# Kernel optimization log

Measured on AMD Instinct MI355X. Metric: run time of the kernel, lower is better.

Reference implementation:

```python
import jax, jax.numpy as jnp
import numpy as np

N = 50000        # nodes
E = 1600000      # edges (avg degree 32)
N_IN = 128       # atomic embedding dim
N_F = 128        # filter dim
N_G = 50         # gaussian basis size for fij
CUTOFF = 5.0


def setup_inputs() -> dict:
    key = jax.random.key(0)
    ks = jax.random.split(key, 12)
    feat = jax.random.normal(ks[0], (N, N_IN), jnp.float32)
    fij = jax.random.uniform(ks[1], (E, N_G), dtype=jnp.float32)
    rij = jax.random.uniform(ks[2], (E,), dtype=jnp.float32) * CUTOFF
    src = jax.random.randint(ks[3], (E,), 0, N, dtype=jnp.int32)
    dst = jax.random.randint(ks[4], (E,), 0, N, dtype=jnp.int32)

    def w(k, shape, fan_in):
        return jax.random.normal(k, shape, jnp.float32) / np.float32(np.sqrt(fan_in))

    W_in2f = w(ks[5], (N_IN, N_F), N_IN)                 # Dense(n_in, n_filters, bias=False)
    Wf1 = w(ks[6], (N_G, N_F), N_G); bf1 = jnp.zeros((N_F,), jnp.float32)   # filter_network layer 1 (swish)
    Wf2 = w(ks[7], (N_F, N_F), N_F); bf2 = jnp.zeros((N_F,), jnp.float32)   # filter_network layer 2
    Wm1 = w(ks[8], (N_F, N_IN), N_F); bm1 = jnp.zeros((N_IN,), jnp.float32) # msg_transform layer 1 (swish)
    Wm2 = w(ks[9], (N_IN, N_IN), N_IN); bm2 = jnp.zeros((N_IN,), jnp.float32)
    return dict(feat=feat, fij=fij, rij=rij, src=src, dst=dst,
                W_in2f=W_in2f, Wf1=Wf1, bf1=bf1, Wf2=Wf2, bf2=bf2,
                Wm1=Wm1, bm1=bm1, Wm2=Wm2, bm2=bm2)


def _swish(x):
    return x * jax.nn.sigmoid(x)


def reference(feat, fij, rij, src, dst, W_in2f, Wf1, bf1, Wf2, bf2, Wm1, bm1, Wm2, bm2):
    # Cosine cutoff: 0.5*(cos(pi*r/rc)+1) for r < rc, else 0
    C = 0.5 * (jnp.cos(jnp.pi * rij / CUTOFF) + 1.0) * (rij < CUTOFF).astype(rij.dtype)
    # Edge filters: filter_network(fij) * C  -> [E, n_filters]
    he = (_swish(fij @ Wf1 + bf1) @ Wf2 + bf2) * C[:, None]
    # Node features projected: in2f(feat) -> [N, n_filters]
    hv = feat @ W_in2f
    # u_mul_e: gather source node feature, multiply by edge filter -> [E, n_filters]
    m = hv[src] * he
    # aggregator: sum messages at destination nodes -> [N, n_filters]
    agg = jax.ops.segment_sum(m, dst, num_segments=N)
    # msg_transform: Dense(swish) -> Dense
    return _swish(agg @ Wm1 + bm1) @ Wm2 + bm2
```

## Files before the change

### kernel.cpp

```cpp
#include <hip/hip_runtime.h>

#define N_NODES 50000
#define N_EDGES 1600000

typedef _Float16 f16x8 __attribute__((ext_vector_type(8)));
typedef float f32x4 __attribute__((ext_vector_type(4)));

__global__ void prep_weights(const float* __restrict__ Wf1,
                             const float* __restrict__ Wf2,
                             _Float16* __restrict__ W1img,
                             _Float16* __restrict__ W2img) {
    int i = blockIdx.x * 256 + threadIdx.x;
    if (i < 8192) {
        int n = i >> 6, k = i & 63;
        float v = (k < 50) ? Wf1[k * 128 + n] : 0.0f;
        W1img[n * 64 + (((k >> 3) ^ (n & 7)) << 3) + (k & 7)] = (_Float16)v;
    }
    if (i < 16384) {
        int n = i >> 7, k = i & 127;
        W2img[n * 128 + (((k >> 3) ^ (n & 7)) << 3) + (k & 7)] =
            (_Float16)Wf2[k * 128 + n];
    }
}

__global__ void hist_kernel(const int* __restrict__ dstv, int* __restrict__ cnt) {
    int e = blockIdx.x * 256 + threadIdx.x;
    if (e < N_EDGES) atomicAdd(&cnt[dstv[e]], 1);
}

__global__ __launch_bounds__(1024) void scan_reduce(const int* __restrict__ cnt,
                                                    int* __restrict__ bsum) {
    __shared__ int ws[16];
    int tid = threadIdx.x, lane = tid & 63;
    int i = blockIdx.x * 1024 + tid;
    int x = (i < N_NODES) ? cnt[i] : 0;
    for (int o = 32; o > 0; o >>= 1) x += __shfl_down(x, o);
    if (lane == 0) ws[tid >> 6] = x;
    __syncthreads();
    if (tid == 0) {
        int s = 0;
        for (int w = 0; w < 16; ++w) s += ws[w];
        bsum[blockIdx.x] = s;
    }
}

__global__ void scan_top(int* __restrict__ bsum) {
    if (threadIdx.x == 0) {
        int s = 0;
        for (int b = 0; b < 49; ++b) { int v = bsum[b]; bsum[b] = s; s += v; }
    }
}

__global__ __launch_bounds__(1024) void scan_apply(int* __restrict__ cnt,
                                                   const int* __restrict__ bsum) {
    __shared__ int ws[16], wo[16];
    int tid = threadIdx.x, lane = tid & 63, wid = tid >> 6;
    int i = blockIdx.x * 1024 + tid;
    int x = (i < N_NODES) ? cnt[i] : 0;
    int incl = x;
    for (int o = 1; o < 64; o <<= 1) {
        int y = __shfl_up(incl, o);
        if (lane >= o) incl += y;
    }
    if (lane == 63) ws[wid] = incl;
    __syncthreads();
    if (tid == 0) {
        int s = 0;
        for (int w = 0; w < 16; ++w) { wo[w] = s; s += ws[w]; }
    }
    __syncthreads();
    if (i < N_NODES) cnt[i] = bsum[blockIdx.x] + wo[wid] + incl - x;
}

__global__ void scatter_kernel(const int* __restrict__ dstv,
                               const int* __restrict__ srcv,
                               const float* __restrict__ rij,
                               int* __restrict__ cursor,
                               int4* __restrict__ meta) {
    int e = blockIdx.x * 256 + threadIdx.x;
    if (e < N_EDGES) {
        int d = dstv[e];
        int pos = atomicAdd(&cursor[d], 1);
        meta[pos] = make_int4(e, srcv[e], d, __float_as_int(rij[e]));
    }
}

__global__ __launch_bounds__(256) void hv_kernel(const float* __restrict__ feat,
                                                 const float* __restrict__ W,
                                                 _Float16* __restrict__ hvh) {
    __shared__ float sAT[128 * 20];
    const int tid = threadIdx.x;
    const int row0 = blockIdx.x * 16;
    for (int t = 0; t < 8; ++t) {
        int flat = tid + 256 * t;
        int rr = flat >> 7, k = flat & 127;
        sAT[k * 20 + rr] = feat[(row0 + rr) * 128 + k];
    }
    __syncthreads();
    const int c = tid & 127, rh = tid >> 7;
    float acc[8] = {0, 0, 0, 0, 0, 0, 0, 0};
    for (int k = 0; k < 128; ++k) {
        float wval = W[k * 128 + c];
        const float4 alo = *(const float4*)&sAT[k * 20 + rh * 8];
        const float4 ahi = *(const float4*)&sAT[k * 20 + rh * 8 + 4];
        acc[0] += alo.x * wval; acc[1] += alo.y * wval;
        acc[2] += alo.z * wval; acc[3] += alo.w * wval;
        acc[4] += ahi.x * wval; acc[5] += ahi.y * wval;
        acc[6] += ahi.z * wval; acc[7] += ahi.w * wval;
    }
    for (int r = 0; r < 8; ++r)
        hvh[(row0 + rh * 8 + r) * 128 + c] = (_Float16)acc[r];
}

__global__ __launch_bounds__(512, 4) void edge_kernel(
        const float* __restrict__ fij, const _Float16* __restrict__ hvh,
        const _Float16* __restrict__ W1img, const _Float16* __restrict__ W2img,
        const float* __restrict__ bf1, const float* __restrict__ bf2,
        const int4* __restrict__ meta, float* __restrict__ agg) {
    __shared__ __align__(16) char smem[65536];
    __shared__ __align__(16) int4 sMeta[128];
    _Float16* sW1 = (_Float16*)smem;
    _Float16* sW2 = (_Float16*)(smem + 16384);
    _Float16* sT0 = (_Float16*)smem;
    _Float16* sT1 = (_Float16*)(smem + 49152);
    _Float16* sM  = (_Float16*)(smem + 16384);

    const int tid = threadIdx.x;
    const int lane = tid & 63;
    const int wv = tid >> 6;
    const int l15 = lane & 15;
    const int q = lane >> 4;
    const int e0 = blockIdx.x * 128;

    const int arow = wv * 16 + l15;
    const int eid = meta[e0 + arow].x;
    const float* frow = fij + (long)eid * 50;
    float2 p0 = *(const float2*)(frow + q * 8 + 0);
    float2 p1 = *(const float2*)(frow + q * 8 + 2);
    float2 p2 = *(const float2*)(frow + q * 8 + 4);
    float2 p3 = *(const float2*)(frow + q * 8 + 6);
    const int kb = 32 + q * 8;
    float2 z2 = make_float2(0.f, 0.f);
    float2 p4 = (kb + 1 < 50) ? *(const float2*)(frow + kb + 0) : z2;
    float2 p5 = (kb + 3 < 50) ? *(const float2*)(frow + kb + 2) : z2;
    float2 p6 = (kb + 5 < 50) ? *(const float2*)(frow + kb + 4) : z2;
    float2 p7 = (kb + 7 < 50) ? *(const float2*)(frow + kb + 6) : z2;
    f16x8 a0, a1;
    a0[0] = (_Float16)p0.x; a0[1] = (_Float16)p0.y;
    a0[2] = (_Float16)p1.x; a0[3] = (_Float16)p1.y;
    a0[4] = (_Float16)p2.x; a0[5] = (_Float16)p2.y;
    a0[6] = (_Float16)p3.x; a0[7] = (_Float16)p3.y;
    a1[0] = (_Float16)p4.x; a1[1] = (_Float16)p4.y;
    a1[2] = (_Float16)p5.x; a1[3] = (_Float16)p5.y;
    a1[4] = (_Float16)p6.x; a1[5] = (_Float16)p6.y;
    a1[6] = (_Float16)p7.x; a1[7] = (_Float16)p7.y;

    if (tid < 128) sMeta[tid] = meta[e0 + tid];
    {
        const float4* s1 = (const float4*)W1img;
        float4* d1 = (float4*)sW1;
        d1[tid] = s1[tid]; d1[tid + 512] = s1[tid + 512];
        const float4* s2 = (const float4*)W2img;
        float4* d2 = (float4*)sW2;
        for (int t = 0; t < 4; ++t) d2[tid + 512 * t] = s2[tid + 512 * t];
    }
    float b1v[8], b2v[8];
    for (int nb = 0; nb < 8; ++nb) {
        b1v[nb] = bf1[nb * 16 + l15];
        b2v[nb] = bf2[nb * 16 + l15];
    }
    __syncthreads();

    const int col2 = tid & 63;
    const int rseg0 = (tid >> 6) * 16;
    unsigned int pf[16];
    #pragma unroll
    for (int i = 0; i < 16; ++i) {
        long srcn = sMeta[rseg0 + i].y;
        pf[i] = *(const unsigned int*)(hvh + srcn * 128 + col2 * 2);
    }

    f32x4 acc[8];
    for (int nb = 0; nb < 8; ++nb) acc[nb] = (f32x4){0.f, 0.f, 0.f, 0.f};
    {
        f16x8 b[8];
        for (int nb = 0; nb < 8; ++nb) {
            int n = nb * 16 + l15;
            b[nb] = *(const f16x8*)&sW1[n * 64 + ((q ^ (n & 7)) << 3)];
        }
        for (int nb = 0; nb < 8; ++nb)
            acc[nb] = __builtin_amdgcn_mfma_f32_16x16x32_f16(a0, b[nb], acc[nb], 0, 0, 0);
        for (int nb = 0; nb < 8; ++nb) {
            int n = nb * 16 + l15;
            b[nb] = *(const f16x8*)&sW1[n * 64 + (((4 + q) ^ (n & 7)) << 3)];
        }
        for (int nb = 0; nb < 8; ++nb)
            acc[nb] = __builtin_amdgcn_mfma_f32_16x16x32_f16(a1, b[nb], acc[nb], 0, 0, 0);
    }
    __syncthreads();

    for (int nb = 0; nb < 8; ++nb)
        for (int r = 0; r < 4; ++r) {
            float x = acc[nb][r] + b1v[nb];
            float tt = x / (1.0f + __expf(-x));
            int row = wv * 16 + q * 4 + r;
            int col = nb * 16 + l15;
            _Float16* base = (row < 64) ? sT0 + row * 128 : sT1 + (row - 64) * 128;
            base[(((col >> 3) ^ (row & 7)) << 3) + (col & 7)] = (_Float16)tt;
        }
    __syncthreads();

    for (int nb = 0; nb < 8; ++nb) acc[nb] = (f32x4){0.f, 0.f, 0.f, 0.f};
    {
        const int row = wv * 16 + l15;
        const _Float16* abase = (row < 64) ? sT0 + row * 128 : sT1 + (row - 64) * 128;
        for (int ks = 0; ks < 4; ++ks) {
            int c = ks * 4 + q;
            f16x8 a = *(const f16x8*)&abase[(c ^ (row & 7)) << 3];
            for (int nb = 0; nb < 8; ++nb) {
                int n = nb * 16 + l15;
                f16x8 b = *(const f16x8*)&sW2[n * 128 + ((c ^ (n & 7)) << 3)];
                acc[nb] = __builtin_amdgcn_mfma_f32_16x16x32_f16(a, b, acc[nb], 0, 0, 0);
            }
        }
    }
    __syncthreads();

    for (int r = 0; r < 4; ++r) {
        int row = wv * 16 + q * 4 + r;
        float rv = __int_as_float(sMeta[row].w);
        float Cr = (rv < 5.0f) ? 0.5f * (__cosf(0.6283185307179586f * rv) + 1.0f) : 0.0f;
        for (int nb = 0; nb < 8; ++nb) {
            int col = nb * 16 + l15;
            sM[row * 132 + col] = (_Float16)((acc[nb][r] + b2v[nb]) * Cr);
        }
    }
    __syncthreads();

    {
        float run0 = 0.0f, run1 = 0.0f;
        int cur = sMeta[rseg0].z;
        #pragma unroll
        for (int i = 0; i < 16; ++i) {
            int r = rseg0 + i;
            int d = sMeta[r].z;
            if (d != cur) {
                atomicAdd(&agg[cur * 128 + col2 * 2], run0);
                atomicAdd(&agg[cur * 128 + col2 * 2 + 1], run1);
                run0 = 0.0f; run1 = 0.0f; cur = d;
            }
            union { unsigned int u; _Float16 h[2]; } hv2; hv2.u = pf[i];
            union { unsigned int u; _Float16 h[2]; } m2;
            m2.u = *(const unsigned int*)&sM[r * 132 + col2 * 2];
            run0 += (float)hv2.h[0] * (float)m2.h[0];
            run1 += (float)hv2.h[1] * (float)m2.h[1];
        }
        atomicAdd(&agg[cur * 128 + col2 * 2], run0);
        atomicAdd(&agg[cur * 128 + col2 * 2 + 1], run1);
    }
}

__global__ __launch_bounds__(256) void out_kernel(const float* __restrict__ agg,
                                                  const float* __restrict__ Wm1,
                                                  const float* __restrict__ bm1,
                                                  const float* __restrict__ Wm2,
                                                  const float* __restrict__ bm2,
                                                  float* __restrict__ out) {
    __shared__ float sAT[128 * 20];
    __shared__ float sTT[128 * 20];
    const int tid = threadIdx.x;
    const int row0 = blockIdx.x * 16;
    for (int t = 0; t < 8; ++t) {
        int flat = tid + 256 * t;
        int rr = flat >> 7, k = flat & 127;
        sAT[k * 20 + rr] = agg[(row0 + rr) * 128 + k];
    }
    __syncthreads();
    const int c = tid & 127, rh = tid >> 7;
    float acc[8] = {0, 0, 0, 0, 0, 0, 0, 0};
    for (int k = 0; k < 128; ++k) {
        float wval = Wm1[k * 128 + c];
        const float4 alo = *(const float4*)&sAT[k * 20 + rh * 8];
        const float4 ahi = *(const float4*)&sAT[k * 20 + rh * 8 + 4];
        acc[0] += alo.x * wval; acc[1] += alo.y * wval;
        acc[2] += alo.z * wval; acc[3] += alo.w * wval;
        acc[4] += ahi.x * wval; acc[5] += ahi.y * wval;
        acc[6] += ahi.z * wval; acc[7] += ahi.w * wval;
    }
    float bm1c = bm1[c];
    for (int r = 0; r < 8; ++r) {
        float x = acc[r] + bm1c;
        sTT[c * 20 + rh * 8 + r] = x / (1.0f + __expf(-x));
    }
    __syncthreads();
    float acc2[8] = {0, 0, 0, 0, 0, 0, 0, 0};
    for (int k = 0; k < 128; ++k) {
        float wval = Wm2[k * 128 + c];
        const float4 alo = *(const float4*)&sTT[k * 20 + rh * 8];
        const float4 ahi = *(const float4*)&sTT[k * 20 + rh * 8 + 4];
        acc2[0] += alo.x * wval; acc2[1] += alo.y * wval;
        acc2[2] += alo.z * wval; acc2[3] += alo.w * wval;
        acc2[4] += ahi.x * wval; acc2[5] += ahi.y * wval;
        acc2[6] += ahi.z * wval; acc2[7] += ahi.w * wval;
    }
    float bm2c = bm2[c];
    for (int r = 0; r < 8; ++r)
        out[(row0 + rh * 8 + r) * 128 + c] = acc2[r] + bm2c;
}

extern "C" void kernel_launch(void* const* d_in, const int* in_sizes, int n_in,
                              void* d_out, int out_size, void* d_ws, size_t ws_size,
                              hipStream_t stream) {
    const float* feat   = (const float*)d_in[0];
    const float* fij    = (const float*)d_in[1];
    const float* rij    = (const float*)d_in[2];
    const int*   srcv   = (const int*)d_in[3];
    const int*   dstv   = (const int*)d_in[4];
    const float* W_in2f = (const float*)d_in[5];
    const float* Wf1    = (const float*)d_in[6];
    const float* bf1    = (const float*)d_in[7];
    const float* Wf2    = (const float*)d_in[8];
    const float* bf2    = (const float*)d_in[9];
    const float* Wm1    = (const float*)d_in[10];
    const float* bm1    = (const float*)d_in[11];
    const float* Wm2    = (const float*)d_in[12];
    const float* bm2    = (const float*)d_in[13];
    float* out = (float*)d_out;

    char* ws = (char*)d_ws;
    float*    agg   = (float*)ws;
    _Float16* hvh   = (_Float16*)(ws + 25600000);
    int4*     meta  = (int4*)(ws + 38400000);
    int*      cnt   = (int*)(ws + 64000000);
    int*      bsum  = (int*)(ws + 64200000);
    _Float16* W1img = (_Float16*)(ws + 64200704);
    _Float16* W2img = (_Float16*)(ws + 64217088);

    hipMemsetAsync(agg, 0, (size_t)N_NODES * 128 * sizeof(float), stream);
    hipMemsetAsync(cnt, 0, (size_t)N_NODES * sizeof(int), stream);
    prep_weights<<<64, 256, 0, stream>>>(Wf1, Wf2, W1img, W2img);
    hv_kernel<<<3125, 256, 0, stream>>>(feat, W_in2f, hvh);
    hist_kernel<<<(N_EDGES + 255) / 256, 256, 0, stream>>>(dstv, cnt);
    scan_reduce<<<49, 1024, 0, stream>>>(cnt, bsum);
    scan_top<<<1, 64, 0, stream>>>(bsum);
    scan_apply<<<49, 1024, 0, stream>>>(cnt, bsum);
    scatter_kernel<<<(N_EDGES + 255) / 256, 256, 0, stream>>>(dstv, srcv, rij, cnt, meta);
    edge_kernel<<<12500, 512, 0, stream>>>(fij, hvh, W1img, W2img, bf1, bf2, meta, agg);
    out_kernel<<<3125, 256, 0, stream>>>(agg, Wm1, bm1, Wm2, bm2, out);
}
```

Before: 954.6 us.

## Make edge kernel persistent over five tiles with prefetch of next tile

The edge kernel now processes five 128-edge tiles per block (2500 blocks instead of 12500), loading weights once and software-pipelining the next tile's metadata, fij rows and hv gathers behind the current tile's MFMAs. The scatter pass writes only edge ids instead of int4 metadata, with src/dst/rij gathered inside the edge kernel. Message staging reuses the swizzled layout, and swish uses a hardware reciprocal. The aim is to amortise the weight load and hide gather latency, at the cost of more registers and extra barriers, plus indirect gathers of src/dst/rij.

```diff
diff --git a/kernel.cpp b/kernel.cpp
--- a/kernel.cpp
+++ b/kernel.cpp
@@ -5,6 +5,14 @@
 
 typedef _Float16 f16x8 __attribute__((ext_vector_type(8)));
 typedef float f32x4 __attribute__((ext_vector_type(4)));
+
+__device__ __forceinline__ float fast_rcp(float v) {
+#if __has_builtin(__builtin_amdgcn_rcpf)
+    return __builtin_amdgcn_rcpf(v);
+#else
+    return __frcp_rn(v);
+#endif
+}
 
 __global__ void prep_weights(const float* __restrict__ Wf1,
                              const float* __restrict__ Wf2,
@@ -73,15 +81,13 @@
 }
 
 __global__ void scatter_kernel(const int* __restrict__ dstv,
-                               const int* __restrict__ srcv,
-                               const float* __restrict__ rij,
                                int* __restrict__ cursor,
-                               int4* __restrict__ meta) {
+                               int* __restrict__ eids) {
     int e = blockIdx.x * 256 + threadIdx.x;
     if (e < N_EDGES) {
         int d = dstv[e];
         int pos = atomicAdd(&cursor[d], 1);
-        meta[pos] = make_int4(e, srcv[e], d, __float_as_int(rij[e]));
+        eids[pos] = e;
     }
 }
 
@@ -116,35 +122,55 @@
         const float* __restrict__ fij, const _Float16* __restrict__ hvh,
         const _Float16* __restrict__ W1img, const _Float16* __restrict__ W2img,
         const float* __restrict__ bf1, const float* __restrict__ bf2,
-        const int4* __restrict__ meta, float* __restrict__ agg) {
+        const int* __restrict__ eids, const int* __restrict__ srcv,
+        const int* __restrict__ dstv, const float* __restrict__ rij,
+        float* __restrict__ agg) {
     __shared__ __align__(16) char smem[65536];
-    __shared__ __align__(16) int4 sMeta[128];
+    __shared__ __align__(16) int4 sMeta[2][128];
     _Float16* sW1 = (_Float16*)smem;
     _Float16* sW2 = (_Float16*)(smem + 16384);
-    _Float16* sT0 = (_Float16*)smem;
-    _Float16* sT1 = (_Float16*)(smem + 49152);
-    _Float16* sM  = (_Float16*)(smem + 16384);
+    _Float16* sX0 = (_Float16*)smem;
+    _Float16* sX1 = (_Float16*)(smem + 49152);
 
     const int tid = threadIdx.x;
     const int lane = tid & 63;
     const int wv = tid >> 6;
     const int l15 = lane & 15;
     const int q = lane >> 4;
-    const int e0 = blockIdx.x * 128;
-
+    const int col2 = tid & 63;
+    const int rseg0 = wv * 16;
     const int arow = wv * 16 + l15;
-    const int eid = meta[e0 + arow].x;
+
+    long e0 = (long)blockIdx.x * 640;
+
+    const int kb = 32 + q * 8;
+    const float2 z2 = make_float2(0.f, 0.f);
+    int eid = eids[e0 + arow];
     const float* frow = fij + (long)eid * 50;
     float2 p0 = *(const float2*)(frow + q * 8 + 0);
     float2 p1 = *(const float2*)(frow + q * 8 + 2);
     float2 p2 = *(const float2*)(frow + q * 8 + 4);
     float2 p3 = *(const float2*)(frow + q * 8 + 6);
-    const int kb = 32 + q * 8;
-    float2 z2 = make_float2(0.f, 0.f);
     float2 p4 = (kb + 1 < 50) ? *(const float2*)(frow + kb + 0) : z2;
     float2 p5 = (kb + 3 < 50) ? *(const float2*)(frow + kb + 2) : z2;
     float2 p6 = (kb + 5 < 50) ? *(const float2*)(frow + kb + 4) : z2;
     float2 p7 = (kb + 7 < 50) ? *(const float2*)(frow + kb + 6) : z2;
+
+    if (tid < 128) {
+        int e = eids[e0 + tid];
+        sMeta[0][tid] = make_int4(e, srcv[e], dstv[e], __float_as_int(rij[e]));
+    }
+    const float4* g1 = (const float4*)W1img;
+    const float4* g2 = (const float4*)W2img;
+    float4* d1 = (float4*)sW1;
+    float4* d2 = (float4*)sW2;
+    d1[tid] = g1[tid]; d1[tid + 512] = g1[tid + 512];
+    for (int u = 0; u < 4; ++u) d2[tid + 512 * u] = g2[tid + 512 * u];
+    float b1v[8], b2v[8];
+    for (int nb = 0; nb < 8; ++nb) {
+        b1v[nb] = bf1[nb * 16 + l15];
+        b2v[nb] = bf2[nb * 16 + l15];
+    }
     f16x8 a0, a1;
     a0[0] = (_Float16)p0.x; a0[1] = (_Float16)p0.y;
     a0[2] = (_Float16)p1.x; a0[3] = (_Float16)p1.y;
@@ -154,109 +180,160 @@
     a1[2] = (_Float16)p5.x; a1[3] = (_Float16)p5.y;
     a1[4] = (_Float16)p6.x; a1[5] = (_Float16)p6.y;
     a1[6] = (_Float16)p7.x; a1[7] = (_Float16)p7.y;
-
-    if (tid < 128) sMeta[tid] = meta[e0 + tid];
-    {
-        const float4* s1 = (const float4*)W1img;
-        float4* d1 = (float4*)sW1;
-        d1[tid] = s1[tid]; d1[tid + 512] = s1[tid + 512];
-        const float4* s2 = (const float4*)W2img;
-        float4* d2 = (float4*)sW2;
-        for (int t = 0; t < 4; ++t) d2[tid + 512 * t] = s2[tid + 512 * t];
-    }
-    float b1v[8], b2v[8];
-    for (int nb = 0; nb < 8; ++nb) {
-        b1v[nb] = bf1[nb * 16 + l15];
-        b2v[nb] = bf2[nb * 16 + l15];
-    }
-    __syncthreads();
-
-    const int col2 = tid & 63;
-    const int rseg0 = (tid >> 6) * 16;
+    __syncthreads();
+
     unsigned int pf[16];
     #pragma unroll
     for (int i = 0; i < 16; ++i) {
-        long srcn = sMeta[rseg0 + i].y;
+        long srcn = sMeta[0][rseg0 + i].y;
         pf[i] = *(const unsigned int*)(hvh + srcn * 128 + col2 * 2);
     }
 
-    f32x4 acc[8];
-    for (int nb = 0; nb < 8; ++nb) acc[nb] = (f32x4){0.f, 0.f, 0.f, 0.f};
-    {
-        f16x8 b[8];
-        for (int nb = 0; nb < 8; ++nb) {
-            int n = nb * 16 + l15;
-            b[nb] = *(const f16x8*)&sW1[n * 64 + ((q ^ (n & 7)) << 3)];
-        }
-        for (int nb = 0; nb < 8; ++nb)
-            acc[nb] = __builtin_amdgcn_mfma_f32_16x16x32_f16(a0, b[nb], acc[nb], 0, 0, 0);
-        for (int nb = 0; nb < 8; ++nb) {
-            int n = nb * 16 + l15;
-            b[nb] = *(const f16x8*)&sW1[n * 64 + (((4 + q) ^ (n & 7)) << 3)];
-        }
-        for (int nb = 0; nb < 8; ++nb)
-            acc[nb] = __builtin_amdgcn_mfma_f32_16x16x32_f16(a1, b[nb], acc[nb], 0, 0, 0);
-    }
-    __syncthreads();
-
-    for (int nb = 0; nb < 8; ++nb)
-        for (int r = 0; r < 4; ++r) {
-            float x = acc[nb][r] + b1v[nb];
-            float tt = x / (1.0f + __expf(-x));
-            int row = wv * 16 + q * 4 + r;
-            int col = nb * 16 + l15;
-            _Float16* base = (row < 64) ? sT0 + row * 128 : sT1 + (row - 64) * 128;
-            base[(((col >> 3) ^ (row & 7)) << 3) + (col & 7)] = (_Float16)tt;
-        }
-    __syncthreads();
-
-    for (int nb = 0; nb < 8; ++nb) acc[nb] = (f32x4){0.f, 0.f, 0.f, 0.f};
-    {
-        const int row = wv * 16 + l15;
-        const _Float16* abase = (row < 64) ? sT0 + row * 128 : sT1 + (row - 64) * 128;
-        for (int ks = 0; ks < 4; ++ks) {
-            int c = ks * 4 + q;
-            f16x8 a = *(const f16x8*)&abase[(c ^ (row & 7)) << 3];
+    for (int t = 0; t < 5; ++t) {
+        const int4* sMc = sMeta[t & 1];
+        int4* sMn = sMeta[(t + 1) & 1];
+        const bool more = (t < 4);
+        const long e0n = e0 + 128;
+
+        f32x4 acc[8];
+        for (int nb = 0; nb < 8; ++nb) acc[nb] = (f32x4){0.f, 0.f, 0.f, 0.f};
+        {
+            f16x8 b[8];
             for (int nb = 0; nb < 8; ++nb) {
                 int n = nb * 16 + l15;
-                f16x8 b = *(const f16x8*)&sW2[n * 128 + ((c ^ (n & 7)) << 3)];
-                acc[nb] = __builtin_amdgcn_mfma_f32_16x16x32_f16(a, b, acc[nb], 0, 0, 0);
-            }
-        }
-    }
-    __syncthreads();
-
-    for (int r = 0; r < 4; ++r) {
-        int row = wv * 16 + q * 4 + r;
-        float rv = __int_as_float(sMeta[row].w);
-        float Cr = (rv < 5.0f) ? 0.5f * (__cosf(0.6283185307179586f * rv) + 1.0f) : 0.0f;
-        for (int nb = 0; nb < 8; ++nb) {
-            int col = nb * 16 + l15;
-            sM[row * 132 + col] = (_Float16)((acc[nb][r] + b2v[nb]) * Cr);
-        }
-    }
-    __syncthreads();
-
-    {
-        float run0 = 0.0f, run1 = 0.0f;
-        int cur = sMeta[rseg0].z;
+                b[nb] = *(const f16x8*)&sW1[n * 64 + ((q ^ (n & 7)) << 3)];
+            }
+            for (int nb = 0; nb < 8; ++nb)
+                acc[nb] = __builtin_amdgcn_mfma_f32_16x16x32_f16(a0, b[nb], acc[nb], 0, 0, 0);
+            for (int nb = 0; nb < 8; ++nb) {
+                int n = nb * 16 + l15;
+                b[nb] = *(const f16x8*)&sW1[n * 64 + (((4 + q) ^ (n & 7)) << 3)];
+            }
+            for (int nb = 0; nb < 8; ++nb)
+                acc[nb] = __builtin_amdgcn_mfma_f32_16x16x32_f16(a1, b[nb], acc[nb], 0, 0, 0);
+        }
+        __syncthreads();
+
+        int4 mN = make_int4(0, 0, 0, 0);
+        int eidN = 0;
+        if (more) {
+            if (tid < 128) {
+                int e = eids[e0n + tid];
+                mN = make_int4(e, srcv[e], dstv[e], __float_as_int(rij[e]));
+            }
+            eidN = eids[e0n + arow];
+        }
+
         #pragma unroll
-        for (int i = 0; i < 16; ++i) {
-            int r = rseg0 + i;
-            int d = sMeta[r].z;
-            if (d != cur) {
-                atomicAdd(&agg[cur * 128 + col2 * 2], run0);
-                atomicAdd(&agg[cur * 128 + col2 * 2 + 1], run1);
-                run0 = 0.0f; run1 = 0.0f; cur = d;
-            }
-            union { unsigned int u; _Float16 h[2]; } hv2; hv2.u = pf[i];
-            union { unsigned int u; _Float16 h[2]; } m2;
-            m2.u = *(const unsigned int*)&sM[r * 132 + col2 * 2];
-            run0 += (float)hv2.h[0] * (float)m2.h[0];
-            run1 += (float)hv2.h[1] * (float)m2.h[1];
-        }
-        atomicAdd(&agg[cur * 128 + col2 * 2], run0);
-        atomicAdd(&agg[cur * 128 + col2 * 2 + 1], run1);
+        for (int nb = 0; nb < 8; ++nb)
+            #pragma unroll
+            for (int r = 0; r < 4; ++r) {
+                float x = acc[nb][r] + b1v[nb];
+                float tt = x * fast_rcp(1.0f + __expf(-x));
+                int row = wv * 16 + q * 4 + r;
+                int col = nb * 16 + l15;
+                _Float16* base = (row < 64) ? sX0 + row * 128 : sX1 + (row - 64) * 128;
+                base[(((col >> 3) ^ (row & 7)) << 3) + (col & 7)] = (_Float16)tt;
+            }
+        float2 n0, n1, n2, n3, n4, n5, n6, n7;
+        if (more) {
+            const float* frn = fij + (long)eidN * 50;
+            n0 = *(const float2*)(frn + q * 8 + 0);
+            n1 = *(const float2*)(frn + q * 8 + 2);
+            n2 = *(const float2*)(frn + q * 8 + 4);
+            n3 = *(const float2*)(frn + q * 8 + 6);
+            n4 = (kb + 1 < 50) ? *(const float2*)(frn + kb + 0) : z2;
+            n5 = (kb + 3 < 50) ? *(const float2*)(frn + kb + 2) : z2;
+            n6 = (kb + 5 < 50) ? *(const float2*)(frn + kb + 4) : z2;
+            n7 = (kb + 7 < 50) ? *(const float2*)(frn + kb + 6) : z2;
+        }
+        __syncthreads();
+
+        if (more && tid < 128) sMn[tid] = mN;
+
+        for (int nb = 0; nb < 8; ++nb) acc[nb] = (f32x4){0.f, 0.f, 0.f, 0.f};
+        {
+            const int row = wv * 16 + l15;
+            const _Float16* abase = (row < 64) ? sX0 + row * 128 : sX1 + (row - 64) * 128;
+            for (int ks = 0; ks < 4; ++ks) {
+                int c = ks * 4 + q;
+                f16x8 a = *(const f16x8*)&abase[(c ^ (row & 7)) << 3];
+                for (int nb = 0; nb < 8; ++nb) {
+                    int n = nb * 16 + l15;
+                    f16x8 b = *(const f16x8*)&sW2[n * 128 + ((c ^ (n & 7)) << 3)];
+                    acc[nb] = __builtin_amdgcn_mfma_f32_16x16x32_f16(a, b, acc[nb], 0, 0, 0);
+                }
+            }
+        }
+        __syncthreads();
+
+        #pragma unroll
+        for (int r = 0; r < 4; ++r) {
+            int row = wv * 16 + q * 4 + r;
+            float rv = __int_as_float(sMc[row].w);
+            float Cr = (rv < 5.0f) ? 0.5f * (__cosf(0.6283185307179586f * rv) + 1.0f) : 0.0f;
+            #pragma unroll
+            for (int nb = 0; nb < 8; ++nb) {
+                int col = nb * 16 + l15;
+                _Float16* base = (row < 64) ? sX0 + row * 128 : sX1 + (row - 64) * 128;
+                base[(((col >> 3) ^ (row & 7)) << 3) + (col & 7)] =
+                    (_Float16)((acc[nb][r] + b2v[nb]) * Cr);
+            }
+        }
+        f16x8 a0n, a1n;
+        unsigned int pfN[16];
+        float4 w1a, w1b;
+        if (more) {
+            a0n[0] = (_Float16)n0.x; a0n[1] = (_Float16)n0.y;
+            a0n[2] = (_Float16)n1.x; a0n[3] = (_Float16)n1.y;
+            a0n[4] = (_Float16)n2.x; a0n[5] = (_Float16)n2.y;
+            a0n[6] = (_Float16)n3.x; a0n[7] = (_Float16)n3.y;
+            a1n[0] = (_Float16)n4.x; a1n[1] = (_Float16)n4.y;
+            a1n[2] = (_Float16)n5.x; a1n[3] = (_Float16)n5.y;
+            a1n[4] = (_Float16)n6.x; a1n[5] = (_Float16)n6.y;
+            a1n[6] = (_Float16)n7.x; a1n[7] = (_Float16)n7.y;
+            #pragma unroll
+            for (int i = 0; i < 16; ++i) {
+                long srcn = sMn[rseg0 + i].y;
+                pfN[i] = *(const unsigned int*)(hvh + srcn * 128 + col2 * 2);
+            }
+            w1a = g1[tid]; w1b = g1[tid + 512];
+        }
+        __syncthreads();
+
+        {
+            const _Float16* rb = (rseg0 < 64) ? sX0 + rseg0 * 128
+                                              : sX1 + (rseg0 - 64) * 128;
+            float run0 = 0.0f, run1 = 0.0f;
+            int cur = sMc[rseg0].z;
+            #pragma unroll
+            for (int i = 0; i < 16; ++i) {
+                int d = sMc[rseg0 + i].z;
+                if (d != cur) {
+                    atomicAdd(&agg[(long)cur * 128 + col2 * 2], run0);
+                    atomicAdd(&agg[(long)cur * 128 + col2 * 2 + 1], run1);
+                    run0 = 0.0f; run1 = 0.0f; cur = d;
+                }
+                union { unsigned int u; _Float16 h[2]; } hv2; hv2.u = pf[i];
+                union { unsigned int u; _Float16 h[2]; } m2;
+                m2.u = *(const unsigned int*)
+                    &rb[i * 128 + ((((col2 >> 2) ^ (i & 7)) << 3) | ((col2 & 3) << 1))];
+                run0 += (float)hv2.h[0] * (float)m2.h[0];
+                run1 += (float)hv2.h[1] * (float)m2.h[1];
+            }
+            atomicAdd(&agg[(long)cur * 128 + col2 * 2], run0);
+            atomicAdd(&agg[(long)cur * 128 + col2 * 2 + 1], run1);
+        }
+
+        if (more) {
+            __syncthreads();
+            d1[tid] = w1a; d1[tid + 512] = w1b;
+            a0 = a0n; a1 = a1n;
+            #pragma unroll
+            for (int i = 0; i < 16; ++i) pf[i] = pfN[i];
+            e0 = e0n;
+            __syncthreads();
+        }
     }
 }
 
@@ -290,7 +367,7 @@
     float bm1c = bm1[c];
     for (int r = 0; r < 8; ++r) {
         float x = acc[r] + bm1c;
-        sTT[c * 20 + rh * 8 + r] = x / (1.0f + __expf(-x));
+        sTT[c * 20 + rh * 8 + r] = x * fast_rcp(1.0f + __expf(-x));
     }
     __syncthreads();
     float acc2[8] = {0, 0, 0, 0, 0, 0, 0, 0};
@@ -330,7 +407,7 @@
     char* ws = (char*)d_ws;
     float*    agg   = (float*)ws;
     _Float16* hvh   = (_Float16*)(ws + 25600000);
-    int4*     meta  = (int4*)(ws + 38400000);
+    int*      eids  = (int*)(ws + 38400000);
     int*      cnt   = (int*)(ws + 64000000);
     int*      bsum  = (int*)(ws + 64200000);
     _Float16* W1img = (_Float16*)(ws + 64200704);
@@ -344,7 +421,8 @@
     scan_reduce<<<49, 1024, 0, stream>>>(cnt, bsum);
     scan_top<<<1, 64, 0, stream>>>(bsum);
     scan_apply<<<49, 1024, 0, stream>>>(cnt, bsum);
-    scatter_kernel<<<(N_EDGES + 255) / 256, 256, 0, stream>>>(dstv, srcv, rij, cnt, meta);
-    edge_kernel<<<12500, 512, 0, stream>>>(fij, hvh, W1img, W2img, bf1, bf2, meta, agg);
+    scatter_kernel<<<(N_EDGES + 255) / 256, 256, 0, stream>>>(dstv, cnt, eids);
+    edge_kernel<<<2500, 512, 0, stream>>>(fij, hvh, W1img, W2img, bf1, bf2,
+                                          eids, srcv, dstv, rij, agg);
     out_kernel<<<3125, 256, 0, stream>>>(agg, Wm1, bm1, Wm2, bm2, out);
 }
```

After: 1.600 ms. 1.68x slower.

## Move node-side GEMMs to MFMA fp16 and fuse hv projection with histogram

Applied to the files above, without the earlier changes.

The fp32 scalar-FMA hv projection and the two output MLP layers are replaced with fp16 MFMA 16x16x32 tiles, using swizzled fp16 weight images prepared up front. The hv GEMM and the destination-degree histogram are merged into one launch to cut a kernel boundary. Swish division becomes a fast reciprocal in both the edge and output kernels. Inputs and intermediates are rounded to fp16 (agg in particular), which lowers precision and risks overflow when aggregated values are large.

```diff
diff --git a/kernel.cpp b/kernel.cpp
--- a/kernel.cpp
+++ b/kernel.cpp
@@ -6,10 +6,24 @@
 typedef _Float16 f16x8 __attribute__((ext_vector_type(8)));
 typedef float f32x4 __attribute__((ext_vector_type(4)));
 
+__device__ __forceinline__ float fast_rcp(float v) {
+#if __has_builtin(__builtin_amdgcn_rcpf)
+    return __builtin_amdgcn_rcpf(v);
+#else
+    return __frcp_rn(v);
+#endif
+}
+
 __global__ void prep_weights(const float* __restrict__ Wf1,
                              const float* __restrict__ Wf2,
+                             const float* __restrict__ W_in2f,
+                             const float* __restrict__ Wm1,
+                             const float* __restrict__ Wm2,
                              _Float16* __restrict__ W1img,
-                             _Float16* __restrict__ W2img) {
+                             _Float16* __restrict__ W2img,
+                             _Float16* __restrict__ Wi2fimg,
+                             _Float16* __restrict__ Wm1img,
+                             _Float16* __restrict__ Wm2img) {
     int i = blockIdx.x * 256 + threadIdx.x;
     if (i < 8192) {
         int n = i >> 6, k = i & 63;
@@ -18,14 +32,65 @@
     }
     if (i < 16384) {
         int n = i >> 7, k = i & 127;
-        W2img[n * 128 + (((k >> 3) ^ (n & 7)) << 3) + (k & 7)] =
-            (_Float16)Wf2[k * 128 + n];
-    }
-}
-
-__global__ void hist_kernel(const int* __restrict__ dstv, int* __restrict__ cnt) {
-    int e = blockIdx.x * 256 + threadIdx.x;
-    if (e < N_EDGES) atomicAdd(&cnt[dstv[e]], 1);
+        int off = n * 128 + (((k >> 3) ^ (n & 7)) << 3) + (k & 7);
+        int src = k * 128 + n;
+        W2img[off]   = (_Float16)Wf2[src];
+        Wi2fimg[off] = (_Float16)W_in2f[src];
+        Wm1img[off]  = (_Float16)Wm1[src];
+        Wm2img[off]  = (_Float16)Wm2[src];
+    }
+}
+
+__global__ __launch_bounds__(512) void fused_hv_hist(
+        const float* __restrict__ feat, const _Float16* __restrict__ Wi2fimg,
+        _Float16* __restrict__ hvh,
+        const int* __restrict__ dstv, int* __restrict__ cnt) {
+    const int b = blockIdx.x;
+    const int tid = threadIdx.x;
+    if (b < 391) {
+        const int lane = tid & 63, wv = tid >> 6;
+        const int l15 = lane & 15, q = lane >> 4;
+        const int row0 = b * 128;
+        int ar = row0 + wv * 16 + l15;
+        if (ar > N_NODES - 1) ar = N_NODES - 1;
+        const float* arow = feat + (long)ar * 128;
+        f16x8 a[4];
+        #pragma unroll
+        for (int ks = 0; ks < 4; ++ks) {
+            const float* p = arow + ks * 32 + q * 8;
+            float2 u0 = *(const float2*)(p + 0);
+            float2 u1 = *(const float2*)(p + 2);
+            float2 u2 = *(const float2*)(p + 4);
+            float2 u3 = *(const float2*)(p + 6);
+            a[ks][0] = (_Float16)u0.x; a[ks][1] = (_Float16)u0.y;
+            a[ks][2] = (_Float16)u1.x; a[ks][3] = (_Float16)u1.y;
+            a[ks][4] = (_Float16)u2.x; a[ks][5] = (_Float16)u2.y;
+            a[ks][6] = (_Float16)u3.x; a[ks][7] = (_Float16)u3.y;
+        }
+        f32x4 acc[8];
+        for (int nb = 0; nb < 8; ++nb) acc[nb] = (f32x4){0.f, 0.f, 0.f, 0.f};
+        #pragma unroll
+        for (int ks = 0; ks < 4; ++ks) {
+            int c = ks * 4 + q;
+            #pragma unroll
+            for (int nb = 0; nb < 8; ++nb) {
+                int n = nb * 16 + l15;
+                f16x8 bf = *(const f16x8*)&Wi2fimg[n * 128 + ((c ^ (n & 7)) << 3)];
+                acc[nb] = __builtin_amdgcn_mfma_f32_16x16x32_f16(a[ks], bf, acc[nb], 0, 0, 0);
+            }
+        }
+        #pragma unroll
+        for (int nb = 0; nb < 8; ++nb)
+            #pragma unroll
+            for (int r = 0; r < 4; ++r) {
+                int orow = row0 + wv * 16 + q * 4 + r;
+                if (orow < N_NODES)
+                    hvh[(long)orow * 128 + nb * 16 + l15] = (_Float16)acc[nb][r];
+            }
+    } else {
+        int e = (b - 391) * 512 + tid;
+        if (e < N_EDGES) atomicAdd(&cnt[dstv[e]], 1);
+    }
 }
 
 __global__ __launch_bounds__(1024) void scan_reduce(const int* __restrict__ cnt,
@@ -83,33 +148,6 @@
         int pos = atomicAdd(&cursor[d], 1);
         meta[pos] = make_int4(e, srcv[e], d, __float_as_int(rij[e]));
     }
-}
-
-__global__ __launch_bounds__(256) void hv_kernel(const float* __restrict__ feat,
-                                                 const float* __restrict__ W,
-                                                 _Float16* __restrict__ hvh) {
-    __shared__ float sAT[128 * 20];
-    const int tid = threadIdx.x;
-    const int row0 = blockIdx.x * 16;
-    for (int t = 0; t < 8; ++t) {
-        int flat = tid + 256 * t;
-        int rr = flat >> 7, k = flat & 127;
-        sAT[k * 20 + rr] = feat[(row0 + rr) * 128 + k];
-    }
-    __syncthreads();
-    const int c = tid & 127, rh = tid >> 7;
-    float acc[8] = {0, 0, 0, 0, 0, 0, 0, 0};
-    for (int k = 0; k < 128; ++k) {
-        float wval = W[k * 128 + c];
-        const float4 alo = *(const float4*)&sAT[k * 20 + rh * 8];
-        const float4 ahi = *(const float4*)&sAT[k * 20 + rh * 8 + 4];
-        acc[0] += alo.x * wval; acc[1] += alo.y * wval;
-        acc[2] += alo.z * wval; acc[3] += alo.w * wval;
-        acc[4] += ahi.x * wval; acc[5] += ahi.y * wval;
-        acc[6] += ahi.z * wval; acc[7] += ahi.w * wval;
-    }
-    for (int r = 0; r < 8; ++r)
-        hvh[(row0 + rh * 8 + r) * 128 + c] = (_Float16)acc[r];
 }
 
 __global__ __launch_bounds__(512, 4) void edge_kernel(
@@ -202,7 +240,7 @@
     for (int nb = 0; nb < 8; ++nb)
         for (int r = 0; r < 4; ++r) {
             float x = acc[nb][r] + b1v[nb];
-            float tt = x / (1.0f + __expf(-x));
+            float tt = x * fast_rcp(1.0f + __expf(-x));
             int row = wv * 16 + q * 4 + r;
             int col = nb * 16 + l15;
             _Float16* base = (row < 64) ? sT0 + row * 128 : sT1 + (row - 64) * 128;
@@ -260,52 +298,84 @@
     }
 }
 
-__global__ __launch_bounds__(256) void out_kernel(const float* __restrict__ agg,
-                                                  const float* __restrict__ Wm1,
+__global__ __launch_bounds__(512) void out_kernel(const float* __restrict__ agg,
+                                                  const _Float16* __restrict__ Wm1img,
                                                   const float* __restrict__ bm1,
-                                                  const float* __restrict__ Wm2,
+                                                  const _Float16* __restrict__ Wm2img,
                                                   const float* __restrict__ bm2,
                                                   float* __restrict__ out) {
-    __shared__ float sAT[128 * 20];
-    __shared__ float sTT[128 * 20];
-    const int tid = threadIdx.x;
-    const int row0 = blockIdx.x * 16;
-    for (int t = 0; t < 8; ++t) {
-        int flat = tid + 256 * t;
-        int rr = flat >> 7, k = flat & 127;
-        sAT[k * 20 + rr] = agg[(row0 + rr) * 128 + k];
-    }
-    __syncthreads();
-    const int c = tid & 127, rh = tid >> 7;
-    float acc[8] = {0, 0, 0, 0, 0, 0, 0, 0};
-    for (int k = 0; k < 128; ++k) {
-        float wval = Wm1[k * 128 + c];
-        const float4 alo = *(const float4*)&sAT[k * 20 + rh * 8];
-        const float4 ahi = *(const float4*)&sAT[k * 20 + rh * 8 + 4];
-        acc[0] += alo.x * wval; acc[1] += alo.y * wval;
-        acc[2] += alo.z * wval; acc[3] += alo.w * wval;
-        acc[4] += ahi.x * wval; acc[5] += ahi.y * wval;
-        acc[6] += ahi.z * wval; acc[7] += ahi.w * wval;
-    }
-    float bm1c = bm1[c];
-    for (int r = 0; r < 8; ++r) {
-        float x = acc[r] + bm1c;
-        sTT[c * 20 + rh * 8 + r] = x / (1.0f + __expf(-x));
-    }
-    __syncthreads();
-    float acc2[8] = {0, 0, 0, 0, 0, 0, 0, 0};
-    for (int k = 0; k < 128; ++k) {
-        float wval = Wm2[k * 128 + c];
-        const float4 alo = *(const float4*)&sTT[k * 20 + rh * 8];
-        const float4 ahi = *(const float4*)&sTT[k * 20 + rh * 8 + 4];
-        acc2[0] += alo.x * wval; acc2[1] += alo.y * wval;
-        acc2[2] += alo.z * wval; acc2[3] += alo.w * wval;
-        acc2[4] += ahi.x * wval; acc2[5] += ahi.y * wval;
-        acc2[6] += ahi.z * wval; acc2[7] += ahi.w * wval;
-    }
-    float bm2c = bm2[c];
-    for (int r = 0; r < 8; ++r)
-        out[(row0 + rh * 8 + r) * 128 + c] = acc2[r] + bm2c;
+    __shared__ __align__(16) _Float16 sT[128 * 128];
+    const int tid = threadIdx.x, lane = tid & 63, wv = tid >> 6;
+    const int l15 = lane & 15, q = lane >> 4;
+    const int row0 = blockIdx.x * 128;
+    int ar = row0 + wv * 16 + l15;
+    if (ar > N_NODES - 1) ar = N_NODES - 1;
+    const float* arow = agg + (long)ar * 128;
+    f16x8 a[4];
+    #pragma unroll
+    for (int ks = 0; ks < 4; ++ks) {
+        const float* p = arow + ks * 32 + q * 8;
+        float2 u0 = *(const float2*)(p + 0);
+        float2 u1 = *(const float2*)(p + 2);
+        float2 u2 = *(const float2*)(p + 4);
+        float2 u3 = *(const float2*)(p + 6);
+        a[ks][0] = (_Float16)u0.x; a[ks][1] = (_Float16)u0.y;
+        a[ks][2] = (_Float16)u1.x; a[ks][3] = (_Float16)u1.y;
+        a[ks][4] = (_Float16)u2.x; a[ks][5] = (_Float16)u2.y;
+        a[ks][6] = (_Float16)u3.x; a[ks][7] = (_Float16)u3.y;
+    }
+    float b1v[8], b2v[8];
+    for (int nb = 0; nb < 8; ++nb) {
+        b1v[nb] = bm1[nb * 16 + l15];
+        b2v[nb] = bm2[nb * 16 + l15];
+    }
+    f32x4 acc[8];
+    for (int nb = 0; nb < 8; ++nb) acc[nb] = (f32x4){0.f, 0.f, 0.f, 0.f};
+    #pragma unroll
+    for (int ks = 0; ks < 4; ++ks) {
+        int c = ks * 4 + q;
+        #pragma unroll
+        for (int nb = 0; nb < 8; ++nb) {
+            int n = nb * 16 + l15;
+            f16x8 bf = *(const f16x8*)&Wm1img[n * 128 + ((c ^ (n & 7)) << 3)];
+            acc[nb] = __builtin_amdgcn_mfma_f32_16x16x32_f16(a[ks], bf, acc[nb], 0, 0, 0);
+        }
+    }
+    #pragma unroll
+    for (int nb = 0; nb < 8; ++nb)
+        #pragma unroll
+        for (int r = 0; r < 4; ++r) {
+            float x = acc[nb][r] + b1v[nb];
+            float tt = x * fast_rcp(1.0f + __expf(-x));
+            int row = wv * 16 + q * 4 + r;
+            int col = nb * 16 + l15;
+            sT[row * 128 + (((col >> 3) ^ (row & 7)) << 3) + (col & 7)] = (_Float16)tt;
+        }
+    __syncthreads();
+    for (int nb = 0; nb < 8; ++nb) acc[nb] = (f32x4){0.f, 0.f, 0.f, 0.f};
+    {
+        const int rowA = wv * 16 + l15;
+        const _Float16* abase = &sT[rowA * 128];
+        #pragma unroll
+        for (int ks = 0; ks < 4; ++ks) {
+            int c = ks * 4 + q;
+            f16x8 a2 = *(const f16x8*)&abase[(c ^ (rowA & 7)) << 3];
+            #pragma unroll
+            for (int nb = 0; nb < 8; ++nb) {
+                int n = nb * 16 + l15;
+                f16x8 bf = *(const f16x8*)&Wm2img[n * 128 + ((c ^ (n & 7)) << 3)];
+                acc[nb] = __builtin_amdgcn_mfma_f32_16x16x32_f16(a2, bf, acc[nb], 0, 0, 0);
+            }
+        }
+    }
+    #pragma unroll
+    for (int nb = 0; nb < 8; ++nb)
+        #pragma unroll
+        for (int r = 0; r < 4; ++r) {
+            int orow = row0 + wv * 16 + q * 4 + r;
+            if (orow < N_NODES)
+                out[(long)orow * 128 + nb * 16 + l15] = acc[nb][r] + b2v[nb];
+        }
 }
 
 extern "C" void kernel_launch(void* const* d_in, const int* in_sizes, int n_in,
@@ -328,23 +398,26 @@
     float* out = (float*)d_out;
 
     char* ws = (char*)d_ws;
-    float*    agg   = (float*)ws;
-    _Float16* hvh   = (_Float16*)(ws + 25600000);
-    int4*     meta  = (int4*)(ws + 38400000);
-    int*      cnt   = (int*)(ws + 64000000);
-    int*      bsum  = (int*)(ws + 64200000);
-    _Float16* W1img = (_Float16*)(ws + 64200704);
-    _Float16* W2img = (_Float16*)(ws + 64217088);
+    float*    agg     = (float*)ws;
+    _Float16* hvh     = (_Float16*)(ws + 25600000);
+    int4*     meta    = (int4*)(ws + 38400000);
+    int*      cnt     = (int*)(ws + 64000000);
+    int*      bsum    = (int*)(ws + 64200000);
+    _Float16* W1img   = (_Float16*)(ws + 64200704);
+    _Float16* W2img   = (_Float16*)(ws + 64217088);
+    _Float16* Wi2fimg = (_Float16*)(ws + 64249856);
+    _Float16* Wm1img  = (_Float16*)(ws + 64282624);
+    _Float16* Wm2img  = (_Float16*)(ws + 64315392);
 
     hipMemsetAsync(agg, 0, (size_t)N_NODES * 128 * sizeof(float), stream);
     hipMemsetAsync(cnt, 0, (size_t)N_NODES * sizeof(int), stream);
-    prep_weights<<<64, 256, 0, stream>>>(Wf1, Wf2, W1img, W2img);
-    hv_kernel<<<3125, 256, 0, stream>>>(feat, W_in2f, hvh);
-    hist_kernel<<<(N_EDGES + 255) / 256, 256, 0, stream>>>(dstv, cnt);
+    prep_weights<<<64, 256, 0, stream>>>(Wf1, Wf2, W_in2f, Wm1, Wm2,
+                                         W1img, W2img, Wi2fimg, Wm1img, Wm2img);
+    fused_hv_hist<<<391 + 3125, 512, 0, stream>>>(feat, Wi2fimg, hvh, dstv, cnt);
     scan_reduce<<<49, 1024, 0, stream>>>(cnt, bsum);
     scan_top<<<1, 64, 0, stream>>>(bsum);
     scan_apply<<<49, 1024, 0, stream>>>(cnt, bsum);
     scatter_kernel<<<(N_EDGES + 255) / 256, 256, 0, stream>>>(dstv, srcv, rij, cnt, meta);
     edge_kernel<<<12500, 512, 0, stream>>>(fij, hvh, W1img, W2img, bf1, bf2, meta, agg);
-    out_kernel<<<3125, 256, 0, stream>>>(agg, Wm1, bm1, Wm2, bm2, out);
-}
+    out_kernel<<<391, 512, 0, stream>>>(agg, Wm1img, bm1, Wm2img, bm2, out);
+}
```

New measurement: 871.7 us. -8.7%, faster.
